# Kernel optimization log

Hardware: AMD Instinct MI355X
Metric: run time of the kernel (lower is better)

The kernel has to match this reference:

```python
import jax, jax.numpy as jnp
import numpy as np

KERNEL_SIZE = 9
HEAD_SIZE = 64


def setup_inputs() -> dict:
    key = jax.random.key(0)
    k1, k2 = jax.random.split(key)
    B, S, D = 8, 4096, 768          # hidden = num_heads(12) * head_size(64)
    H = D // HEAD_SIZE              # 12 heads
    inputs = jax.random.normal(k1, (B, S, D), dtype=jnp.float32)
    filters = jax.random.normal(k2, (B, S, H * KERNEL_SIZE), dtype=jnp.float32)
    return {"inputs": inputs, "filters": filters}


def reference(inputs, filters):
    k = KERNEL_SIZE
    hd = HEAD_SIZE
    bs, S, d = inputs.shape
    H = d // hd
    pad = k // 2
    # softmax-normalized per-(position, head) kernels: [B, S, H, k]
    f = jax.nn.softmax(filters.reshape(bs, S, H, k), axis=-1)
    # 'same' padding along sequence, then gather sliding windows (im2col)
    x = jnp.pad(inputs, ((0, 0), (pad, pad), (0, 0)))        # [B, S+k-1, d]
    idx = jnp.arange(S)[:, None] + jnp.arange(k)[None, :]     # [S, k]
    win = x[:, idx].reshape(bs, S, k, H, hd)                  # [B, S, k, H, hd]
    # dynamic depthwise conv: contract kernel taps per head
    out = jnp.einsum('bskhd,bshk->bshd', win, f)              # [B, S, H, hd]
    return out
```

## Files before the change

kernel.cpp:

```cpp
#include <hip/hip_runtime.h>
#include <math.h>


#define KS 9
#define HD 64
#define NH 12
#define DMODEL 768
#define SEQ 4096
#define BATCH 8
#define TTILE 16
#define NROWS (TTILE + KS - 1)
#define CHUNKS (SEQ / TTILE)
#define FSTRIDE (NH * KS)
#define NTHREADS 192

__global__ __launch_bounds__(NTHREADS, 4) void lightconv_kernel(
    const float* __restrict__ x,
    const float* __restrict__ filt,
    float* __restrict__ out)
{
    __shared__ float wlds[TTILE * FSTRIDE];

    const int blk   = blockIdx.x;
    const int chunk = blk & (CHUNKS - 1);
    const int b     = blk >> 8;
    const int s0    = chunk * TTILE;
    const int t     = threadIdx.x;
    const int head  = t >> 4;
    const int d4    = (t & 15) << 2;

    const float4 zero = make_float4(0.f, 0.f, 0.f, 0.f);

    const float* fbase = filt + ((size_t)b * SEQ + s0) * FSTRIDE;
    float freg[KS];
#pragma unroll
    for (int i = 0; i < KS; ++i) freg[i] = fbase[t + i * NTHREADS];

    const float* xc = x + (size_t)b * SEQ * DMODEL + head * HD + d4;
    float4 rows[NROWS];
#pragma unroll
    for (int r = 0; r < NROWS; ++r) {
        const int ss = s0 + r - (KS / 2);
        rows[r] = (ss >= 0 && ss < SEQ)
                    ? *reinterpret_cast<const float4*>(xc + (size_t)ss * DMODEL)
                    : zero;
    }

#pragma unroll
    for (int i = 0; i < KS; ++i) wlds[t + i * NTHREADS] = freg[i];
    __syncthreads();

    {
        const int sl = t & 15;
        const int hh = t >> 4;
        float* wp = &wlds[sl * FSTRIDE + hh * KS];
        float w[KS];
        float m = -1e30f;
#pragma unroll
        for (int k = 0; k < KS; ++k) { w[k] = wp[k]; m = fmaxf(m, w[k]); }
        float sum = 0.f;
#pragma unroll
        for (int k = 0; k < KS; ++k) { w[k] = __expf(w[k] - m); sum += w[k]; }
        const float inv = 1.0f / sum;
#pragma unroll
        for (int k = 0; k < KS; ++k) wp[k] = w[k] * inv;
    }
    __syncthreads();

    float* oc = out + (size_t)b * SEQ * DMODEL + head * HD + d4;
#pragma unroll
    for (int i = 0; i < TTILE; ++i) {
        const float* wp = &wlds[i * FSTRIDE + head * KS];
        float4 acc = zero;
#pragma unroll
        for (int k = 0; k < KS; ++k) {
            const float wk = wp[k];
            acc.x += wk * rows[i + k].x;
            acc.y += wk * rows[i + k].y;
            acc.z += wk * rows[i + k].z;
            acc.w += wk * rows[i + k].w;
        }
        *reinterpret_cast<float4*>(oc + (size_t)(s0 + i) * DMODEL) = acc;
    }
}

extern "C" void kernel_launch(void* const* d_in, const int* in_sizes, int n_in,
                              void* d_out, int out_size, void* d_ws, size_t ws_size,
                              hipStream_t stream) {
    const float* x    = (const float*)d_in[0];
    const float* filt = (const float*)d_in[1];
    float* out        = (float*)d_out;

    const int grid = BATCH * CHUNKS;
    lightconv_kernel<<<grid, NTHREADS, 0, stream>>>(x, filt, out);
}
```

Before: 195.1 us.

## Stage input tiles in LDS via direct global-to-LDS loads with head-grouped blocks

Instead of each thread holding a whole sliding window of float4 rows in registers, each block now handles a 4-head slice over a 32-position tile. It loads the input rows straight into shared memory with global_load_lds, one row per wave instruction. Softmax is computed from filter values loaded directly into registers rather than round-tripped through LDS. The larger tile lowers the halo re-read ratio and frees registers, at the cost of more LDS use and LDS reads in the inner loop.

```diff
diff --git a/kernel.cpp b/kernel.cpp
--- a/kernel.cpp
+++ b/kernel.cpp
@@ -8,79 +8,100 @@
 #define DMODEL 768
 #define SEQ 4096
 #define BATCH 8
-#define TTILE 16
+#define TTILE 32
 #define NROWS (TTILE + KS - 1)
+#define HG 4
+#define NHG (NH / HG)
+#define DBLK (HG * HD)
 #define CHUNKS (SEQ / TTILE)
 #define FSTRIDE (NH * KS)
-#define NTHREADS 192
+#define FW (HG * KS)
+#define NTHREADS 256
+#define ROWS_PER_WAVE (NROWS / 4)
 
-__global__ __launch_bounds__(NTHREADS, 4) void lightconv_kernel(
+__global__ __launch_bounds__(NTHREADS, 3) void lightconv_kernel(
     const float* __restrict__ x,
     const float* __restrict__ filt,
     float* __restrict__ out)
 {
-    __shared__ float wlds[TTILE * FSTRIDE];
+    __shared__ float xs[NROWS * DBLK];
+    __shared__ float fwl[TTILE * FW];
 
     const int blk   = blockIdx.x;
     const int chunk = blk & (CHUNKS - 1);
-    const int b     = blk >> 8;
+    const int rest  = blk >> 7;
+    const int hg    = rest % NHG;
+    const int b     = rest / NHG;
     const int s0    = chunk * TTILE;
     const int t     = threadIdx.x;
-    const int head  = t >> 4;
-    const int d4    = (t & 15) << 2;
+    const int wave  = t >> 6;
+    const int lane  = t & 63;
 
-    const float4 zero = make_float4(0.f, 0.f, 0.f, 0.f);
+    float w[KS];
+    if (t < TTILE * HG) {
+        const int sl = t >> 2;
+        const int h  = t & 3;
+        const float* fp = filt + ((size_t)b * SEQ + s0 + sl) * FSTRIDE
+                               + hg * FW + h * KS;
+#pragma unroll
+        for (int k = 0; k < KS; ++k) w[k] = fp[k];
+    }
+    __builtin_amdgcn_sched_barrier(0);
 
-    const float* fbase = filt + ((size_t)b * SEQ + s0) * FSTRIDE;
-    float freg[KS];
+    const float* xrow = x + (size_t)b * SEQ * DMODEL + hg * DBLK + lane * 4;
 #pragma unroll
-    for (int i = 0; i < KS; ++i) freg[i] = fbase[t + i * NTHREADS];
+    for (int j = 0; j < ROWS_PER_WAVE; ++j) {
+        const int r  = wave * ROWS_PER_WAVE + j;
+        const int ss = s0 + r - (KS / 2);
+        if (ss >= 0 && ss < SEQ) {
+            __builtin_amdgcn_global_load_lds(
+                (const __attribute__((address_space(1))) void*)(xrow + (size_t)ss * DMODEL),
+                (__attribute__((address_space(3))) void*)&xs[r * DBLK],
+                16, 0, 0);
+        } else {
+            *reinterpret_cast<float4*>(&xs[r * DBLK + lane * 4]) =
+                make_float4(0.f, 0.f, 0.f, 0.f);
+        }
+    }
+    __builtin_amdgcn_sched_barrier(0);
 
-    const float* xc = x + (size_t)b * SEQ * DMODEL + head * HD + d4;
-    float4 rows[NROWS];
-#pragma unroll
-    for (int r = 0; r < NROWS; ++r) {
-        const int ss = s0 + r - (KS / 2);
-        rows[r] = (ss >= 0 && ss < SEQ)
-                    ? *reinterpret_cast<const float4*>(xc + (size_t)ss * DMODEL)
-                    : zero;
-    }
-
-#pragma unroll
-    for (int i = 0; i < KS; ++i) wlds[t + i * NTHREADS] = freg[i];
-    __syncthreads();
-
-    {
-        const int sl = t & 15;
-        const int hh = t >> 4;
-        float* wp = &wlds[sl * FSTRIDE + hh * KS];
-        float w[KS];
+    if (t < TTILE * HG) {
+        const int sl = t >> 2;
+        const int h  = t & 3;
         float m = -1e30f;
 #pragma unroll
-        for (int k = 0; k < KS; ++k) { w[k] = wp[k]; m = fmaxf(m, w[k]); }
+        for (int k = 0; k < KS; ++k) m = fmaxf(m, w[k]);
         float sum = 0.f;
 #pragma unroll
         for (int k = 0; k < KS; ++k) { w[k] = __expf(w[k] - m); sum += w[k]; }
         const float inv = 1.0f / sum;
+        float* wp = &fwl[sl * FW + h * KS];
 #pragma unroll
         for (int k = 0; k < KS; ++k) wp[k] = w[k] * inv;
     }
+
     __syncthreads();
 
-    float* oc = out + (size_t)b * SEQ * DMODEL + head * HD + d4;
+    const int h    = lane >> 4;
+    const int doff = lane * 4;
+    float* ocol = out + ((size_t)b * SEQ + s0) * DMODEL + hg * DBLK + doff;
+
 #pragma unroll
-    for (int i = 0; i < TTILE; ++i) {
-        const float* wp = &wlds[i * FSTRIDE + head * KS];
-        float4 acc = zero;
+    for (int i = 0; i < TTILE / 4; ++i) {
+        const int sl = wave + i * 4;
+        const float* wp = &fwl[sl * FW + h * KS];
+        float4 a = make_float4(0.f, 0.f, 0.f, 0.f);
 #pragma unroll
         for (int k = 0; k < KS; ++k) {
             const float wk = wp[k];
-            acc.x += wk * rows[i + k].x;
-            acc.y += wk * rows[i + k].y;
-            acc.z += wk * rows[i + k].z;
-            acc.w += wk * rows[i + k].w;
+            const float4 xv = *reinterpret_cast<const float4*>(
+                &xs[(sl + k) * DBLK + doff]);
+            a.x += wk * xv.x;
+            a.y += wk * xv.y;
+            a.z += wk * xv.z;
+            a.w += wk * xv.w;
         }
-        *reinterpret_cast<float4*>(oc + (size_t)(s0 + i) * DMODEL) = acc;
+        *reinterpret_cast<float4*>(ocol + (size_t)sl * DMODEL) = a;
     }
 }
 
@@ -91,6 +112,6 @@
     const float* filt = (const float*)d_in[1];
     float* out        = (float*)d_out;
 
-    const int grid = BATCH * CHUNKS;
+    const int grid = BATCH * NHG * CHUNKS;
     lightconv_kernel<<<grid, NTHREADS, 0, stream>>>(x, filt, out);
 }
```

New measurement: 187.3 us. -4.0%, faster.
